# Performance work log

Measured on AMD Instinct MI355X. Metric: run time of the kernel, lower is better.

Reference implementation:

```python
import jax, jax.numpy as jnp
import numpy as np

BETA = 1.0  # init beta


def l2norm(x, eps=1e-12):
    # matches torch F.normalize(dim=-1)
    n = jnp.sqrt(jnp.sum(x * x, axis=-1, keepdims=True))
    return x / jnp.maximum(n, eps)


def setup_inputs() -> dict:
    key = jax.random.key(0)
    k1, k2 = jax.random.split(key)
    B, T, D, N = 8, 2048, 256, 8192
    z = jax.random.normal(k1, (B, T, D), dtype=jnp.float32)
    # EMA codebook weight (buffer, not trained by grad); l2-normalized as the
    # norm-EMA update keeps it on the unit sphere.
    weight = l2norm(jax.random.normal(k2, (N, D), dtype=jnp.float32))
    return {"z": z, "weight": weight}


def reference(z, weight):
    # z: (B, T, D); weight: (N, D)
    z = l2norm(z)
    zf = z.reshape(-1, z.shape[-1])  # (BT, D)
    # squared L2 distances via expansion: |z|^2 + |w|^2 - 2 z.w
    d = (
        jnp.sum(zf * zf, axis=1, keepdims=True)
        + jnp.sum(weight * weight, axis=1)
        - 2.0 * jnp.einsum("bd,nd->bn", zf, weight)
    )  # (BT, N)
    encoding_indices = jnp.argmin(d, axis=1)  # (BT,)
    z_q = weight[encoding_indices].reshape(z.shape)  # (B, T, D)
    # commitment loss: beta * mse(stop_grad(z_q), z)
    loss = BETA * jnp.mean((jax.lax.stop_gradient(z_q) - z) ** 2)
    # straight-through estimator
    z_q = z + jax.lax.stop_gradient(z_q - z)
    encoding_indices = encoding_indices.reshape(z.shape[:-1])  # (B, T)
    return z_q, loss, encoding_indices
```

## Files before the change

### kernel.cpp

```cpp
#include <hip/hip_runtime.h>
#include <float.h>
#include <math.h>


#define BT_ 16384
#define D_  256
#define N_  8192
#define BETA_ 1.0f

#define BM 128
#define BN 256
#define NKT 8
#define NTILES 32

typedef __attribute__((ext_vector_type(8))) _Float16 f16x8;
typedef __attribute__((ext_vector_type(4))) float f32x4;

__device__ __forceinline__ void gld16(void* lds, const void* g) {
  __builtin_amdgcn_global_load_lds(
      (const __attribute__((address_space(1))) void*)g,
      (__attribute__((address_space(3))) void*)lds, 16, 0, 0);
}

__device__ __forceinline__ unsigned short f2h(float x) {
  _Float16 h = (_Float16)x;
  return __builtin_bit_cast(unsigned short, h);
}
__device__ __forceinline__ float h2f(unsigned short u) {
  return (float)__builtin_bit_cast(_Float16, u);
}
__device__ __forceinline__ unsigned ford(float f) {
  unsigned b = __float_as_uint(f);
  return (b & 0x80000000u) ? ~b : (b | 0x80000000u);
}

__global__ __launch_bounds__(256) void k_prep(const float* __restrict__ z,
                                              const float* __restrict__ w,
                                              float* __restrict__ zn,
                                              ushort* __restrict__ Acat,
                                              float* __restrict__ rl,
                                              float* __restrict__ wn2,
                                              ushort* __restrict__ Bcat) {
  const int b    = blockIdx.x;
  const int lane = threadIdx.x & 63;
  if (b < BT_ / 4) {
    const int row = b * 4 + (threadIdx.x >> 6);
    float4 v = *(reinterpret_cast<const float4*>(z) + (size_t)row * 64 + lane);
    float s = v.x * v.x + v.y * v.y + v.z * v.z + v.w * v.w;
#pragma unroll
    for (int o = 32; o > 0; o >>= 1) s += __shfl_xor(s, o, 64);
    float dn = fmaxf(sqrtf(s), 1e-12f);
    v.x /= dn; v.y /= dn; v.z /= dn; v.w /= dn;
    *(reinterpret_cast<float4*>(zn) + (size_t)row * 64 + lane) = v;
    ushort4 h = make_ushort4(f2h(v.x), f2h(v.y), f2h(v.z), f2h(v.w));
    float lx = v.x - h2f(h.x), ly = v.y - h2f(h.y);
    float lz = v.z - h2f(h.z), lw = v.w - h2f(h.w);
    float s2 = lx * lx + ly * ly + lz * lz + lw * lw;
#pragma unroll
    for (int o = 32; o > 0; o >>= 1) s2 += __shfl_xor(s2, o, 64);
    if (lane == 0) rl[row] = sqrtf(s2);
    reinterpret_cast<ushort4*>(Acat)[(size_t)row * 64 + lane] = h;
  } else {
    const int row = (b - BT_ / 4) * 4 + (threadIdx.x >> 6);
    float4 v = *(reinterpret_cast<const float4*>(w) + (size_t)row * 64 + lane);
    float s = v.x * v.x + v.y * v.y + v.z * v.z + v.w * v.w;
#pragma unroll
    for (int o = 32; o > 0; o >>= 1) s += __shfl_xor(s, o, 64);
    if (lane == 0) wn2[row] = s;
    ushort4 h  = make_ushort4(f2h(v.x), f2h(v.y), f2h(v.z), f2h(v.w));
    ushort4 lo = make_ushort4(f2h(v.x - h2f(h.x)), f2h(v.y - h2f(h.y)),
                              f2h(v.z - h2f(h.z)), f2h(v.w - h2f(h.w)));
    ushort4* B4 = reinterpret_cast<ushort4*>(Bcat);
    size_t rb = (size_t)row * 128 + lane;
    B4[rb]      = h;
    B4[rb + 64] = lo;
  }
}

__global__ __launch_bounds__(512, 4) void k_coarse(const ushort* __restrict__ Acat,
                                                   const ushort* __restrict__ Bcat,
                                                   const float* __restrict__ wn2,
                                                   float* __restrict__ tm,
                                                   float* __restrict__ ts,
                                                   int* __restrict__ ti,
                                                   float* __restrict__ tm2) {
  extern __shared__ char smem[];

  const int tid = threadIdx.x;
  const int l   = tid & 63;
  const int wv  = tid >> 6;
  const int wr  = wv >> 2;
  const int wc  = wv & 3;
  const int bid  = blockIdx.x;
  const int xcd  = bid & 7;
  const int q    = bid >> 3;
  const int chnk = q >> 5, wq = q & 31;
  const int rt   = xcd * 16 + (chnk >> 3) * 8 + (wq >> 2);
  const int ct   = (chnk & 7) * 4 + (wq & 3);
  const int row0 = rt * BM;
  const int col0 = ct * BN;

  const int sgr = ((l & 3) ^ ((l >> 3) & 3)) * 16;
  const char* gsrc[5];
  unsigned    base0[5];
  unsigned    bstr[5];
#pragma unroll
  for (int s = 0; s < 5; ++s) {
    int u = wv * 5 + s;
    if (u < 8) {
      gsrc[s]  = (const char*)Acat + (size_t)(row0 + u * 16 + (l >> 2)) * 512 + sgr;
      base0[s] = u * 1024;
      bstr[s]  = 8192;
    } else if (u < 24) {
      gsrc[s]  = (const char*)Bcat + (size_t)(col0 + (u - 8) * 16 + (l >> 2)) * 1024 + sgr;
      base0[s] = 16384 + (u - 8) * 1024;
      bstr[s]  = 32768;
    } else {
      gsrc[s]  = (const char*)Bcat + (size_t)(col0 + (u - 24) * 16 + (l >> 2)) * 1024 + 512 + sgr;
      base0[s] = 16384 + 16384 + (u - 24) * 1024;
      bstr[s]  = 32768;
    }
  }
#define STAGE(t)                                                               \
  do {                                                                         \
    const unsigned _b = (unsigned)((t) & 1);                                   \
    _Pragma("unroll")                                                          \
    for (int s = 0; s < 5; ++s)                                                \
      gld16(smem + base0[s] + _b * bstr[s], gsrc[s] + (size_t)(t) * 64);       \
  } while (0)

  const int lA  = l & 15;
  const int gk  = (l >> 4) ^ ((lA >> 1) & 3);
  const unsigned aOff  = (unsigned)((wr * 64 + lA) * 64 + gk * 16);
  const unsigned bhOff = (unsigned)(16384 + (wc * 64 + lA) * 64 + gk * 16);

  f32x4 acc[4][4];
#pragma unroll
  for (int i = 0; i < 4; ++i)
#pragma unroll
    for (int j = 0; j < 4; ++j) acc[i][j] = (f32x4){0.f, 0.f, 0.f, 0.f};

  STAGE(0);

  for (int t = 0; t < NKT; ++t) {
    const unsigned ab = (unsigned)((t & 1) * 8192);
    const unsigned bb = (unsigned)((t & 1) * 32768);
    asm volatile("s_waitcnt vmcnt(0)" ::: "memory");
    __builtin_amdgcn_s_barrier();
    __builtin_amdgcn_sched_barrier(0);
    if (t + 1 < NKT) STAGE(t + 1);

    f16x8 af[4], bg[4];
#pragma unroll
    for (int i = 0; i < 4; ++i)
      af[i] = *(const f16x8*)(smem + ab + aOff + i * 1024);
#pragma unroll
    for (int j = 0; j < 4; ++j)
      bg[j] = *(const f16x8*)(smem + bb + bhOff + j * 1024);
    __builtin_amdgcn_s_setprio(1);
#pragma unroll
    for (int i = 0; i < 4; ++i)
#pragma unroll
      for (int j = 0; j < 4; ++j)
        acc[i][j] = __builtin_amdgcn_mfma_f32_16x16x32_f16(af[i], bg[j], acc[i][j], 0, 0, 0);
    __builtin_amdgcn_s_setprio(0);
#pragma unroll
    for (int j = 0; j < 4; ++j)
      bg[j] = *(const f16x8*)(smem + bb + bhOff + 16384 + j * 1024);
    __builtin_amdgcn_s_setprio(1);
#pragma unroll
    for (int i = 0; i < 4; ++i)
#pragma unroll
      for (int j = 0; j < 4; ++j)
        acc[i][j] = __builtin_amdgcn_mfma_f32_16x16x32_f16(af[i], bg[j], acc[i][j], 0, 0, 0);
    __builtin_amdgcn_s_setprio(0);
  }
#undef STAGE

  float wnv[4];
#pragma unroll
  for (int n = 0; n < 4; ++n) wnv[n] = wn2[col0 + wc * 64 + n * 16 + lA];
  float* pm = (float*)smem;
  float* ps = (float*)(smem + 16896);
  int*   pc = (int*)(smem + 33792);
  __syncthreads();

#pragma unroll
  for (int i = 0; i < 4; ++i) {
#pragma unroll
    for (int qq = 0; qq < 4; ++qq) {
      float m = FLT_MAX, s = FLT_MAX; int c = 0;
#pragma unroll
      for (int j = 0; j < 4; ++j) {
        float d = fmaf(-2.0f, acc[i][j][qq], wnv[j]);
        int cc = wc * 64 + j * 16 + lA;
        if (d < m) { s = m; m = d; c = cc; }
        else if (d < s) s = d;
      }
      float om = __shfl_xor(m, 8, 64);
      float os = __shfl_xor(s, 8, 64);
      int   oc = __shfl_xor(c, 8, 64);
      float ns = fminf(fminf(s, os), fmaxf(m, om));
      if (om < m || (om == m && oc < c)) { m = om; c = oc; }
      s = ns;
      if ((l & 8) == 0) {
        int row = wr * 64 + i * 16 + (l >> 4) * 4 + qq;
        int w33 = row * 33 + wc * 8 + (l & 7);
        pm[w33] = m; ps[w33] = s; pc[w33] = c;
      }
    }
  }
  __syncthreads();
  {
    const int row = tid >> 2;
    const int qd  = tid & 3;
    float gm = FLT_MAX, gs = FLT_MAX; int gc = 0x7fffffff;
#pragma unroll
    for (int k = 0; k < 8; ++k) {
      int w33 = row * 33 + qd * 8 + k;
      float m = pm[w33], s = ps[w33]; int c = pc[w33];
      float ns = fminf(fminf(gs, s), fmaxf(gm, m));
      if (m < gm || (m == gm && c < gc)) { gm = m; gc = c; }
      gs = ns;
    }
    tm2[(size_t)(row0 + row) * 128 + ct * 4 + qd] = gm;
#pragma unroll
    for (int msk = 1; msk <= 2; msk <<= 1) {
      float om = __shfl_xor(gm, msk, 64);
      float os = __shfl_xor(gs, msk, 64);
      int   oc = __shfl_xor(gc, msk, 64);
      float ns = fminf(fminf(gs, os), fmaxf(gm, om));
      if (om < gm || (om == gm && oc < gc)) { gm = om; gc = oc; }
      gs = ns;
    }
    if (qd == 0) {
      size_t o = (size_t)ct * BT_ + row0 + row;
      tm[o] = gm; ts[o] = gs; ti[o] = col0 + gc;
    }
  }
}

__global__ __launch_bounds__(256) void k_combine(const float* __restrict__ tm,
                                                 const float* __restrict__ ts,
                                                 const int* __restrict__ ti,
                                                 const float* __restrict__ rl,
                                                 int* __restrict__ idxf,
                                                 float* __restrict__ lim,
                                                 unsigned long long* __restrict__ rowKey,
                                                 int* __restrict__ flagged,
                                                 int* __restrict__ count) {
  const int row = blockIdx.x * 256 + threadIdx.x;
  float m = FLT_MAX, s = FLT_MAX; int bi = 0x7fffffff;
#pragma unroll
  for (int t = 0; t < NTILES; ++t) {
    size_t o = (size_t)t * BT_ + row;
    float om = tm[o], os = ts[o]; int oi = ti[o];
    float nsv = fminf(fminf(s, os), fmaxf(m, om));
    if (om < m || (om == m && oi < bi)) { m = om; bi = oi; }
    s = nsv;
  }
  idxf[row] = bi;
  const float thr = 4.0f * rl[row] + 2.5e-4f;
  if (s - m <= thr) {
    rowKey[row] = ~0ULL;
    lim[row] = m + thr;
    int p = atomicAdd(count, 1);
    flagged[p] = row;
  } else {
    rowKey[row] = 0ULL;
  }
}

__global__ __launch_bounds__(256) void k_refine(const float* __restrict__ zn,
                                                const float* __restrict__ w,
                                                const float* __restrict__ wn2,
                                                const float* __restrict__ tm2,
                                                const float* __restrict__ lim,
                                                const int* __restrict__ flagged,
                                                const int* __restrict__ count,
                                                unsigned long long* __restrict__ rowKey) {
  __shared__ float4 znr[64];
  __shared__ int cand[128];
  __shared__ int ncand;
  const int tid = threadIdx.x;
  const int l   = tid & 63;
  const int wv  = tid >> 6;
  const int cnt = *count;
  for (int f = blockIdx.x; f < cnt; f += gridDim.x) {
    __syncthreads();
    const int row = flagged[f];
    if (tid == 0) ncand = 0;
    if (tid < 64)
      znr[tid] = *(reinterpret_cast<const float4*>(zn) + (size_t)row * 64 + tid);
    __syncthreads();
    const float lv = lim[row];
    if (tid < 128) {
      float t2 = tm2[(size_t)row * 128 + tid];
      if (t2 <= lv) { int p = atomicAdd(&ncand, 1); cand[p] = tid; }
    }
    __syncthreads();
    const int nc = ncand;
    unsigned long long key = ~0ULL;
    for (int i = wv; i < nc; i += 4) {
      const int g = cand[i];
      const int c = g * 64 + l;
      const float4* wr4 = reinterpret_cast<const float4*>(w) + (size_t)c * 64;
      float d0 = 0.f, d1 = 0.f, d2 = 0.f, d3 = 0.f;
#pragma unroll
      for (int k4 = 0; k4 < 16; ++k4) {
        float4 a0 = znr[k4 * 4 + 0], b0 = wr4[k4 * 4 + 0];
        float4 a1 = znr[k4 * 4 + 1], b1 = wr4[k4 * 4 + 1];
        float4 a2 = znr[k4 * 4 + 2], b2 = wr4[k4 * 4 + 2];
        float4 a3 = znr[k4 * 4 + 3], b3 = wr4[k4 * 4 + 3];
        d0 = fmaf(a0.x, b0.x, d0); d0 = fmaf(a0.y, b0.y, d0);
        d0 = fmaf(a0.z, b0.z, d0); d0 = fmaf(a0.w, b0.w, d0);
        d1 = fmaf(a1.x, b1.x, d1); d1 = fmaf(a1.y, b1.y, d1);
        d1 = fmaf(a1.z, b1.z, d1); d1 = fmaf(a1.w, b1.w, d1);
        d2 = fmaf(a2.x, b2.x, d2); d2 = fmaf(a2.y, b2.y, d2);
        d2 = fmaf(a2.z, b2.z, d2); d2 = fmaf(a2.w, b2.w, d2);
        d3 = fmaf(a3.x, b3.x, d3); d3 = fmaf(a3.y, b3.y, d3);
        d3 = fmaf(a3.z, b3.z, d3); d3 = fmaf(a3.w, b3.w, d3);
      }
      float dot = (d0 + d1) + (d2 + d3);
      float d = fmaf(-2.0f, dot, wn2[c]);
      unsigned long long k = ((unsigned long long)ford(d) << 32) | (unsigned)c;
      key = (k < key) ? k : key;
    }
#pragma unroll
    for (int msk = 1; msk < 64; msk <<= 1) {
      unsigned long long ok = __shfl_xor(key, msk, 64);
      key = (ok < key) ? ok : key;
    }
    if (l == 0 && key != ~0ULL) atomicMin(&rowKey[row], key);
  }
}

__global__ __launch_bounds__(256) void k_gather(const float* __restrict__ zn,
                                                const float* __restrict__ w,
                                                const int* __restrict__ idxf,
                                                const unsigned long long* __restrict__ rowKey,
                                                float* __restrict__ zq,
                                                float* __restrict__ idx_out,
                                                float* __restrict__ wpart) {
  const int row  = blockIdx.x * 4 + (threadIdx.x >> 6);
  const int lane = threadIdx.x & 63;
  unsigned long long key = rowKey[row];
  const int bi = (key == 0ULL) ? idxf[row] : (int)(key & 0xFFFFFFFFu);
  float4 cv = *(reinterpret_cast<const float4*>(w)  + (size_t)bi  * 64 + lane);
  float4 zv = *(reinterpret_cast<const float4*>(zn) + (size_t)row * 64 + lane);
  *(reinterpret_cast<float4*>(zq) + (size_t)row * 64 + lane) = cv;
  float dx = cv.x - zv.x, dy = cv.y - zv.y, dz = cv.z - zv.z, dw = cv.w - zv.w;
  float s = dx * dx + dy * dy + dz * dz + dw * dw;
#pragma unroll
  for (int o = 32; o > 0; o >>= 1) s += __shfl_xor(s, o, 64);
  if (lane == 0) {
    wpart[row] = s;
    idx_out[row] = (float)bi;
  }
}

__global__ __launch_bounds__(256) void k_final(const float* __restrict__ wpart,
                                               float* __restrict__ loss_out) {
  __shared__ float wsum[4];
  float s = 0.f;
  for (int i = threadIdx.x; i < BT_; i += 256) s += wpart[i];
#pragma unroll
  for (int o = 32; o > 0; o >>= 1) s += __shfl_xor(s, o, 64);
  if ((threadIdx.x & 63) == 0) wsum[threadIdx.x >> 6] = s;
  __syncthreads();
  if (threadIdx.x == 0)
    loss_out[0] = BETA_ * ((wsum[0] + wsum[1]) + (wsum[2] + wsum[3])) *
                  (1.0f / (float)(BT_ * D_));
}

extern "C" void kernel_launch(void* const* d_in, const int* in_sizes, int n_in,
                              void* d_out, int out_size, void* d_ws, size_t ws_size,
                              hipStream_t stream) {
  const float* z = (const float*)d_in[0];
  const float* w = (const float*)d_in[1];

  float* out      = (float*)d_out;
  float* zq       = out;
  float* loss_out = out + (size_t)BT_ * D_;
  float* idx_out  = loss_out + 1;

  char* wsb = (char*)d_ws;
  float*  zn      = (float*)(wsb);
  ushort* Acat    = (ushort*)(wsb + 16777216);
  ushort* Bcat    = (ushort*)(wsb + 25165824);
  float*  tm      = (float*)(wsb + 33554432);
  float*  ts      = (float*)(wsb + 35651584);
  int*    ti      = (int*)(wsb + 37748736);
  float*  tm2     = (float*)(wsb + 39845888);
  float*  wn2     = (float*)(wsb + 48234496);
  float*  rl      = (float*)(wsb + 48267264);
  int*    idxf    = (int*)(wsb + 48331328);
  float*  lim     = (float*)(wsb + 48396864);
  unsigned long long* rowKey = (unsigned long long*)(wsb + 48462400);
  int*    flagged = (int*)(wsb + 48593472);
  int*    count   = (int*)(wsb + 48659008);
  float*  wpart   = ts;

  hipFuncSetAttribute((const void*)k_coarse,
                      hipFuncAttributeMaxDynamicSharedMemorySize, 81920);

  hipMemsetAsync(count, 0, 4, stream);
  k_prep<<<BT_ / 4 + N_ / 4, 256, 0, stream>>>(z, w, zn, Acat, rl, wn2, Bcat);
  k_coarse<<<(BT_ / BM) * NTILES, 512, 81920, stream>>>(Acat, Bcat, wn2, tm, ts, ti, tm2);
  k_combine<<<BT_ / 256, 256, 0, stream>>>(tm, ts, ti, rl, idxf, lim, rowKey, flagged, count);
  k_refine<<<2048, 256, 0, stream>>>(zn, w, wn2, tm2, lim, flagged, count, rowKey);
  k_gather<<<BT_ / 4, 256, 0, stream>>>(zn, w, idxf, rowKey, zq, idx_out, wpart);
  k_final<<<1, 256, 0, stream>>>(wpart, loss_out);
}
```

Before: 240.3 us.

## Reorder per-wave load assignment and split wait so second B half overlaps compute

Each wave's five async global-to-LDS loads are reassigned so the first three cover the A tile and the first K-half of B, and the last two cover the second K-half of B. The top-of-loop wait now lets the two loads for the second half stay in flight. A new wait plus barrier before the second MFMA batch waits for them. The first half of the MMA work can start before the whole tile lands, at the cost of an extra barrier per iteration. The vmcnt values depend on the compiler issuing the loads in exactly the assumed order.

Result: no change. 241.6 us (+0.5%).

```diff
diff --git a/kernel.cpp b/kernel.cpp
--- a/kernel.cpp
+++ b/kernel.cpp
@@ -104,21 +104,19 @@
   const char* gsrc[5];
   unsigned    base0[5];
   unsigned    bstr[5];
-#pragma unroll
-  for (int s = 0; s < 5; ++s) {
-    int u = wv * 5 + s;
-    if (u < 8) {
-      gsrc[s]  = (const char*)Acat + (size_t)(row0 + u * 16 + (l >> 2)) * 512 + sgr;
-      base0[s] = u * 1024;
-      bstr[s]  = 8192;
-    } else if (u < 24) {
-      gsrc[s]  = (const char*)Bcat + (size_t)(col0 + (u - 8) * 16 + (l >> 2)) * 1024 + sgr;
-      base0[s] = 16384 + (u - 8) * 1024;
-      bstr[s]  = 32768;
-    } else {
-      gsrc[s]  = (const char*)Bcat + (size_t)(col0 + (u - 24) * 16 + (l >> 2)) * 1024 + 512 + sgr;
-      base0[s] = 16384 + 16384 + (u - 24) * 1024;
-      bstr[s]  = 32768;
+  {
+    gsrc[0]  = (const char*)Acat + (size_t)(row0 + wv * 16 + (l >> 2)) * 512 + sgr;
+    base0[0] = wv * 1024;
+    bstr[0]  = 8192;
+#pragma unroll
+    for (int k = 0; k < 2; ++k) {
+      int u = wv * 2 + k;
+      gsrc[1 + k]  = (const char*)Bcat + (size_t)(col0 + u * 16 + (l >> 2)) * 1024 + sgr;
+      base0[1 + k] = 16384 + u * 1024;
+      bstr[1 + k]  = 32768;
+      gsrc[3 + k]  = (const char*)Bcat + (size_t)(col0 + u * 16 + (l >> 2)) * 1024 + 512 + sgr;
+      base0[3 + k] = 32768 + u * 1024;
+      bstr[3 + k]  = 32768;
     }
   }
 #define STAGE(t)                                                               \
@@ -145,7 +143,7 @@
   for (int t = 0; t < NKT; ++t) {
     const unsigned ab = (unsigned)((t & 1) * 8192);
     const unsigned bb = (unsigned)((t & 1) * 32768);
-    asm volatile("s_waitcnt vmcnt(0)" ::: "memory");
+    asm volatile("s_waitcnt vmcnt(2)" ::: "memory");
     __builtin_amdgcn_s_barrier();
     __builtin_amdgcn_sched_barrier(0);
     if (t + 1 < NKT) STAGE(t + 1);
@@ -164,6 +162,12 @@
       for (int j = 0; j < 4; ++j)
         acc[i][j] = __builtin_amdgcn_mfma_f32_16x16x32_f16(af[i], bg[j], acc[i][j], 0, 0, 0);
     __builtin_amdgcn_s_setprio(0);
+    __builtin_amdgcn_sched_barrier(0);
+
+    if (t + 1 < NKT) asm volatile("s_waitcnt vmcnt(5)" ::: "memory");
+    else             asm volatile("s_waitcnt vmcnt(0)" ::: "memory");
+    __builtin_amdgcn_s_barrier();
+    __builtin_amdgcn_sched_barrier(0);
 #pragma unroll
     for (int j = 0; j < 4; ++j)
       bg[j] = *(const f16x8*)(smem + bb + bhOff + 16384 + j * 1024);
```
